# Performance work log

Hardware: AMD Instinct MI355X
Metric: run time of the kernel (lower is better)

The kernel has to match this reference:

```python
import jax, jax.numpy as jnp
import numpy as np

V = 5023   # FLAME vertex count
NJ = 5     # joints: global, neck, jaw, left eye, right eye
PARENTS = [-1, 0, 1, 1, 1]
N_SHAPE, N_EXPR = 100, 50
N_LMK = 68
B = 1024


def batch_rodrigues(rot_vecs):
    # rot_vecs: [N,3] axis-angle -> [N,3,3] rotation matrices
    angle = jnp.linalg.norm(rot_vecs + 1e-8, axis=1, keepdims=True)  # [N,1]
    rot_dir = rot_vecs / angle
    cos = jnp.cos(angle)[:, :, None]  # [N,1,1]
    sin = jnp.sin(angle)[:, :, None]
    rx, ry, rz = rot_dir[:, 0], rot_dir[:, 1], rot_dir[:, 2]
    zeros = jnp.zeros_like(rx)
    K = jnp.stack([zeros, -rz, ry,
                   rz, zeros, -rx,
                   -ry, rx, zeros], axis=1).reshape(-1, 3, 3)
    ident = jnp.eye(3, dtype=rot_vecs.dtype)
    return ident[None] + sin * K + (1.0 - cos) * jnp.matmul(K, K)


def setup_inputs() -> dict:
    key = jax.random.key(0)
    ks = jax.random.split(key, 12)
    shape_params = jax.random.normal(ks[0], (B, N_SHAPE), jnp.float32)
    expression_params = jax.random.normal(ks[1], (B, N_EXPR), jnp.float32)
    pose_params = 0.2 * jax.random.normal(ks[2], (B, 6), jnp.float32)
    land_index = jax.random.randint(ks[3], (N_LMK,), 0, V)
    # buffers / params (stand-ins for the pickled FLAME model)
    v_template = jax.random.normal(ks[4], (V, 3), jnp.float32) * 100.0
    v_template = v_template - jnp.mean(v_template, axis=0, keepdims=True)  # init centering
    shapedirs = jax.random.normal(ks[5], (V, 3, N_SHAPE + N_EXPR), jnp.float32) * 0.1
    posedirs = jax.random.normal(ks[6], ((NJ - 1) * 9, V * 3), jnp.float32) * 0.01
    J_regressor = jax.nn.softmax(jax.random.normal(ks[7], (NJ, V), jnp.float32), axis=1)
    lbs_weights = jax.nn.softmax(jax.random.normal(ks[8], (V, NJ), jnp.float32), axis=1)
    eye_pose = jnp.zeros((1, 6), jnp.float32)
    neck_pose = jnp.zeros((1, 3), jnp.float32)
    return dict(shape_params=shape_params, expression_params=expression_params,
                pose_params=pose_params, land_index=land_index,
                v_template=v_template, shapedirs=shapedirs, posedirs=posedirs,
                J_regressor=J_regressor, lbs_weights=lbs_weights,
                eye_pose=eye_pose, neck_pose=neck_pose)


def lbs(betas, full_pose, v_template, shapedirs, posedirs, J_regressor, lbs_weights):
    b = betas.shape[0]
    # shape/expression blendshapes
    v_shaped = v_template[None] + jnp.einsum('bl,vcl->bvc', betas, shapedirs)  # [B,V,3]
    J = jnp.einsum('jv,bvc->bjc', J_regressor, v_shaped)                       # [B,5,3]
    rot_mats = batch_rodrigues(full_pose.reshape(-1, 3)).reshape(b, NJ, 3, 3)
    ident = jnp.eye(3, dtype=betas.dtype)
    pose_feature = (rot_mats[:, 1:] - ident).reshape(b, -1)                    # [B,36]
    v_posed = v_shaped + jnp.matmul(pose_feature, posedirs).reshape(b, V, 3)
    # rigid transform along kinematic chain
    rel_joints = J.at[:, 1:].add(-J[:, jnp.array(PARENTS[1:])])
    top = jnp.concatenate([rot_mats, rel_joints[..., None]], axis=-1)          # [B,5,3,4]
    bottom = jnp.broadcast_to(jnp.array([0., 0., 0., 1.], betas.dtype), (b, NJ, 1, 4))
    transforms_mat = jnp.concatenate([top, bottom], axis=2)                    # [B,5,4,4]
    chain = [transforms_mat[:, 0]]
    for i in range(1, NJ):
        chain.append(jnp.matmul(chain[PARENTS[i]], transforms_mat[:, i]))
    transforms = jnp.stack(chain, axis=1)                                      # [B,5,4,4]
    posed_joints = transforms[:, :, :3, 3]
    t = jnp.einsum('bnij,bnj->bni', transforms[:, :, :3, :3], J)
    rel_transforms = transforms.at[:, :, :3, 3].add(-t)
    # skinning
    T = jnp.einsum('vj,bjxy->bvxy', lbs_weights, rel_transforms)               # [B,V,4,4]
    verts = jnp.einsum('bvxy,bvy->bvx', T[:, :, :3, :3], v_posed) + T[:, :, :3, 3]
    return verts, posed_joints


def reference(shape_params, expression_params, pose_params, land_index,
              v_template, shapedirs, posedirs, J_regressor, lbs_weights,
              eye_pose, neck_pose):
    b = shape_params.shape[0]
    betas = jnp.concatenate([shape_params, expression_params], axis=1)
    full_pose = jnp.concatenate([pose_params[:, :3],
                                 jnp.broadcast_to(neck_pose, (b, 3)),
                                 pose_params[:, 3:],
                                 jnp.broadcast_to(eye_pose, (b, 6))], axis=1)  # [B,15]
    vertices, _ = lbs(betas, full_pose, v_template, shapedirs, posedirs,
                      J_regressor, lbs_weights)
    landmarks3d = jnp.take(vertices, land_index, axis=1)
    return vertices, landmarks3d
```

## Files before the change

kernel.cpp:

```cpp
#include <hip/hip_runtime.h>

#define V_N 5023
#define V_PAD 5120
#define KTOT 192
#define B_N 1024
#define NC_REAL 15069

#define WS_W     0
#define WS_PART1 5898240
#define WS_PARTJ 6789240
#define WS_JS    6795180
#define WS_JT    6804180
#define WS_A2    5898240
#define WS_RELT  6291456

typedef __attribute__((ext_vector_type(8))) short bf16x8;
typedef __attribute__((ext_vector_type(4))) float f32x4;

__device__ __forceinline__ unsigned short f2bf(float f) {
  union { float f; unsigned int i; } x; x.f = f;
  unsigned int u = x.i;
  u = (u + 0x7FFFu + ((u >> 16) & 1u)) >> 16;
  return (unsigned short)u;
}

__global__ void k_wzero(float4* __restrict__ W4) {
  int g = blockIdx.x * 256 + threadIdx.x;
  W4[g] = make_float4(0.f, 0.f, 0.f, 0.f);
}

__global__ void k_w2a(const float* __restrict__ sd, unsigned int* __restrict__ W32) {
  int g = blockIdx.x * 256 + threadIdx.x;
  if (g >= NC_REAL * 75) return;
  int vc = g / 75, part = g - vc * 75;
  float2 s = *(const float2*)(sd + (size_t)vc * 150 + 2 * part);
  unsigned int w = (unsigned int)f2bf(s.x) | ((unsigned int)f2bf(s.y) << 16);
  int v = vc / 3, c = vc - 3 * v;
  W32[((size_t)c * V_PAD + v) * 96 + part] = w;
}

__global__ void k_w2b(const float* __restrict__ pd, unsigned short* __restrict__ W) {
  __shared__ unsigned short tile[64][38];
  int vc0 = blockIdx.x * 64;
  int t = threadIdx.x;
  for (int i = t; i < 2304; i += 256) {
    int kk = i >> 6, vl = i & 63;
    int vc = vc0 + vl;
    tile[vl][kk] = (vc < NC_REAL) ? f2bf(pd[(size_t)kk * NC_REAL + vc]) : (unsigned short)0;
  }
  __syncthreads();
  for (int i = t; i < 1152; i += 256) {
    int row = i / 18, part = i - row * 18;
    int vc = vc0 + row;
    if (vc < NC_REAL) {
      int v = vc / 3, c = vc - 3 * v;
      unsigned int w = (unsigned int)tile[row][2 * part] |
                       ((unsigned int)tile[row][2 * part + 1] << 16);
      *((unsigned int*)(W + ((size_t)c * V_PAD + v) * KTOT + 152) + part) = w;
    }
  }
}

__global__ void k_js1(const float* __restrict__ jreg, const float* __restrict__ sd,
                      const float* __restrict__ vt,
                      float* __restrict__ part1, float* __restrict__ partJ) {
  int blk = blockIdx.x;
  int vcidx = blk >> 1, kh = blk & 1;
  int t = threadIdx.x;
  int vs = vcidx * 51, ve = vs + 51; if (ve > V_N) ve = V_N;
  if (t < 75) {
    int k = kh * 75 + t;
    float acc[5][3];
    #pragma unroll
    for (int j = 0; j < 5; j++)
      #pragma unroll
      for (int c = 0; c < 3; c++) acc[j][c] = 0.f;
    #pragma unroll 2
    for (int v = vs; v < ve; v++) {
      float jr[5];
      #pragma unroll
      for (int j = 0; j < 5; j++) jr[j] = jreg[j * V_N + v];
      #pragma unroll
      for (int c = 0; c < 3; c++) {
        float s = sd[(size_t)(3 * v + c) * 150 + k];
        #pragma unroll
        for (int j = 0; j < 5; j++) acc[j][c] += jr[j] * s;
      }
    }
    #pragma unroll
    for (int j = 0; j < 5; j++)
      #pragma unroll
      for (int c = 0; c < 3; c++)
        part1[(size_t)vcidx * 2250 + (j * 3 + c) * 150 + kh * 75 + t] = acc[j][c];
  } else if (kh == 0 && t >= 80 && t < 95) {
    int j = (t - 80) / 3, c = (t - 80) % 3;
    float a = 0.f;
    for (int v = vs; v < ve; v++) a += jreg[j * V_N + v] * vt[3 * v + c];
    partJ[vcidx * 15 + (t - 80)] = a;
  }
}

__global__ void k_js2(const float* __restrict__ part1, const float* __restrict__ partJ,
                      float* __restrict__ JS, float* __restrict__ Jt) {
  int blk = blockIdx.x, t = threadIdx.x;
  if (blk < 9) {
    int u = blk * 256 + t;
    if (u < 2250) {
      float s = 0.f;
      #pragma unroll 4
      for (int p = 0; p < 99; p++) s += part1[(size_t)p * 2250 + u];
      JS[u] = s;
    }
  } else if (t < 15) {
    float s = 0.f;
    #pragma unroll 4
    for (int p = 0; p < 99; p++) s += partJ[p * 15 + t];
    Jt[t] = s;
  }
}

__global__ void k_a2(const float* __restrict__ shp, const float* __restrict__ expr,
                     unsigned short* __restrict__ A2) {
  int g = blockIdx.x * 256 + threadIdx.x;
  int b = g / 76, u = g - b * 76;
  int k0 = 2 * u, k1 = 2 * u + 1;
  float f0 = 0.f, f1 = 0.f;
  if (k0 < 100) f0 = shp[b * 100 + k0]; else if (k0 < 150) f0 = expr[b * 50 + k0 - 100];
  if (k1 < 100) f1 = shp[b * 100 + k1]; else if (k1 < 150) f1 = expr[b * 50 + k1 - 100];
  unsigned int w = (unsigned int)f2bf(f0) | ((unsigned int)f2bf(f1) << 16);
  ((unsigned int*)A2)[b * 96 + u] = w;
}

__device__ __forceinline__ void rodrigues(const float* p, float* R) {
  float x = p[0], y = p[1], z = p[2];
  float xa = x + 1e-8f, ya = y + 1e-8f, za = z + 1e-8f;
  float angle = sqrtf(xa * xa + ya * ya + za * za);
  float inv = 1.0f / angle;
  float rx = x * inv, ry = y * inv, rz = z * inv;
  float c = cosf(angle), s = sinf(angle), t1 = 1.0f - c;
  float K[9] = {0.f, -rz, ry, rz, 0.f, -rx, -ry, rx, 0.f};
  float KK[9];
  #pragma unroll
  for (int i = 0; i < 3; i++)
    #pragma unroll
    for (int j = 0; j < 3; j++) {
      float a = 0.f;
      #pragma unroll
      for (int k = 0; k < 3; k++) a += K[i * 3 + k] * K[k * 3 + j];
      KK[i * 3 + j] = a;
    }
  #pragma unroll
  for (int i = 0; i < 9; i++) R[i] = s * K[i] + t1 * KK[i];
  R[0] += 1.f; R[4] += 1.f; R[8] += 1.f;
}

__global__ __launch_bounds__(256) void k_pose(
    const float* __restrict__ pose, const float* __restrict__ neck,
    const float* __restrict__ eye, const float* __restrict__ shp,
    const float* __restrict__ expr, const float* __restrict__ JS,
    const float* __restrict__ Jt, unsigned short* __restrict__ A2,
    float* __restrict__ relT) {
  __shared__ float sBet[150 * 64];
  __shared__ float sJS[2250];
  int t = threadIdx.x;
  int b0 = blockIdx.x * 64;
  for (int i = t; i < 6400; i += 256) {
    int row = i / 100, col = i - row * 100;
    sBet[col * 64 + row] = shp[(size_t)(b0 + row) * 100 + col];
  }
  for (int i = t; i < 3200; i += 256) {
    int row = i / 50, col = i - row * 50;
    sBet[(100 + col) * 64 + row] = expr[(size_t)(b0 + row) * 50 + col];
  }
  for (int i = t; i < 2250; i += 256) sJS[i] = JS[i];
  __syncthreads();
  if (t >= 64) return;
  int b = b0 + t;
  float fp[15];
  fp[0] = pose[b * 6 + 0]; fp[1] = pose[b * 6 + 1]; fp[2] = pose[b * 6 + 2];
  fp[3] = neck[0]; fp[4] = neck[1]; fp[5] = neck[2];
  fp[6] = pose[b * 6 + 3]; fp[7] = pose[b * 6 + 4]; fp[8] = pose[b * 6 + 5];
  #pragma unroll
  for (int i = 0; i < 6; i++) fp[9 + i] = eye[i];
  float R[5][9];
  #pragma unroll
  for (int j = 0; j < 5; j++) rodrigues(&fp[j * 3], R[j]);
  float J[5][3];
  #pragma unroll
  for (int j = 0; j < 5; j++)
    #pragma unroll
    for (int c = 0; c < 3; c++) J[j][c] = Jt[j * 3 + c];
  for (int k = 0; k < 150; k++) {
    float be = sBet[k * 64 + t];
    #pragma unroll
    for (int j = 0; j < 5; j++)
      #pragma unroll
      for (int c = 0; c < 3; c++) J[j][c] += be * sJS[(j * 3 + c) * 150 + k];
  }
  float rel[5][3];
  #pragma unroll
  for (int c = 0; c < 3; c++) {
    rel[0][c] = J[0][c];
    rel[1][c] = J[1][c] - J[0][c];
    rel[2][c] = J[2][c] - J[1][c];
    rel[3][c] = J[3][c] - J[1][c];
    rel[4][c] = J[4][c] - J[1][c];
  }
  float GR[5][9], Gt[5][3];
  #pragma unroll
  for (int i = 0; i < 9; i++) GR[0][i] = R[0][i];
  #pragma unroll
  for (int c = 0; c < 3; c++) Gt[0][c] = rel[0][c];
  const int parent[5] = {0, 0, 1, 1, 1};
  #pragma unroll
  for (int j = 1; j < 5; j++) {
    int p = parent[j];
    #pragma unroll
    for (int r = 0; r < 3; r++)
      #pragma unroll
      for (int c = 0; c < 3; c++) {
        float a = 0.f;
        #pragma unroll
        for (int k = 0; k < 3; k++) a += GR[p][r * 3 + k] * R[j][k * 3 + c];
        GR[j][r * 3 + c] = a;
      }
    #pragma unroll
    for (int r = 0; r < 3; r++) {
      float a = Gt[p][r];
      #pragma unroll
      for (int k = 0; k < 3; k++) a += GR[p][r * 3 + k] * rel[j][k];
      Gt[j][r] = a;
    }
  }
  #pragma unroll
  for (int j = 0; j < 5; j++) {
    #pragma unroll
    for (int r = 0; r < 3; r++) {
      float a = 0.f;
      #pragma unroll
      for (int k = 0; k < 3; k++) a += GR[j][r * 3 + k] * J[j][k];
      float tr = Gt[j][r] - a;
      #pragma unroll
      for (int c = 0; c < 3; c++) relT[b * 60 + j * 12 + r * 4 + c] = GR[j][r * 3 + c];
      relT[b * 60 + j * 12 + r * 4 + 3] = tr;
    }
  }
  #pragma unroll
  for (int j = 1; j < 5; j++)
    #pragma unroll
    for (int r = 0; r < 3; r++)
      #pragma unroll
      for (int c = 0; c < 3; c++) {
        int kk = (j - 1) * 9 + r * 3 + c;
        A2[(size_t)b * KTOT + 152 + kk] = f2bf(R[j][r * 3 + c] - ((r == c) ? 1.f : 0.f));
      }
  #pragma unroll
  for (int kk = 36; kk < 40; kk++) A2[(size_t)b * KTOT + 152 + kk] = 0;
}

__global__ __launch_bounds__(256) void k_mfma(
    const unsigned short* __restrict__ W,
    const unsigned short* __restrict__ A2,
    const float* __restrict__ relT,
    const float* __restrict__ vt,
    const float* __restrict__ lbsw,
    float* __restrict__ out) {
  __shared__ float sRel[64 * 60];
  int t = threadIdx.x;
  int wave = t >> 6, lane = t & 63, ln = lane & 15, quad = lane >> 4;
  int wm = wave >> 1, wn = wave & 1;
  int v0 = blockIdx.x * 128, b0 = blockIdx.y * 64;

  for (int i = t; i < 3840; i += 256) sRel[i] = relT[(size_t)b0 * 60 + i];

  f32x4 acc[3][2][4];
  #pragma unroll
  for (int c = 0; c < 3; c++)
    #pragma unroll
    for (int mt = 0; mt < 2; mt++)
      #pragma unroll
      for (int nt = 0; nt < 4; nt++) {
        acc[c][mt][nt].x = 0.f; acc[c][mt][nt].y = 0.f;
        acc[c][mt][nt].z = 0.f; acc[c][mt][nt].w = 0.f;
      }

  const unsigned short* Abase = A2 + (size_t)(b0 + wm * 32 + ln) * KTOT + quad * 8;
  const unsigned short* Bbase = W + (size_t)(v0 + wn * 64 + ln) * KTOT + quad * 8;

  for (int kc = 0; kc < 6; kc++) {
    bf16x8 af0 = *(const bf16x8*)(Abase + kc * 32);
    bf16x8 af1 = *(const bf16x8*)(Abase + (size_t)16 * KTOT + kc * 32);
    #pragma unroll
    for (int c = 0; c < 3; c++)
      #pragma unroll
      for (int nt = 0; nt < 4; nt++) {
        bf16x8 bfr = *(const bf16x8*)(Bbase + ((size_t)c * V_PAD + nt * 16) * KTOT + kc * 32);
        acc[c][0][nt] = __builtin_amdgcn_mfma_f32_16x16x32_bf16(af0, bfr, acc[c][0][nt], 0, 0, 0);
        acc[c][1][nt] = __builtin_amdgcn_mfma_f32_16x16x32_bf16(af1, bfr, acc[c][1][nt], 0, 0, 0);
      }
  }
  __syncthreads();

  #pragma unroll
  for (int nt = 0; nt < 4; nt++) {
    int v = v0 + wn * 64 + nt * 16 + ln;
    bool ok = v < V_N;
    float vtx = 0.f, vty = 0.f, vtz = 0.f;
    float w5[5] = {0.f, 0.f, 0.f, 0.f, 0.f};
    if (ok) {
      vtx = vt[3 * v]; vty = vt[3 * v + 1]; vtz = vt[3 * v + 2];
      #pragma unroll
      for (int j = 0; j < 5; j++) w5[j] = lbsw[v * 5 + j];
    }
    #pragma unroll
    for (int mt = 0; mt < 2; mt++)
      #pragma unroll
      for (int reg = 0; reg < 4; reg++) {
        int bl = wm * 32 + mt * 16 + quad * 4 + reg;
        float px = acc[0][mt][nt][reg] + vtx;
        float py = acc[1][mt][nt][reg] + vty;
        float pz = acc[2][mt][nt][reg] + vtz;
        float ox = 0.f, oy = 0.f, oz = 0.f;
        const float* M = &sRel[bl * 60];
        #pragma unroll
        for (int j = 0; j < 5; j++) {
          const float* m = M + j * 12;
          float q0 = m[0] * px + m[1] * py + m[2] * pz + m[3];
          float q1 = m[4] * px + m[5] * py + m[6] * pz + m[7];
          float q2 = m[8] * px + m[9] * py + m[10] * pz + m[11];
          ox += w5[j] * q0; oy += w5[j] * q1; oz += w5[j] * q2;
        }
        if (ok) {
          size_t off = (size_t)(b0 + bl) * NC_REAL + (size_t)3 * v;
          out[off] = ox; out[off + 1] = oy; out[off + 2] = oz;
        }
      }
  }
}

__global__ void k_lmk(const float* __restrict__ verts,
                      const int* __restrict__ land,
                      float* __restrict__ lm) {
  int g = blockIdx.x * 256 + threadIdx.x;
  int b = g / 204;
  int r = g - b * 204;
  int i = r / 3, c = r - i * 3;
  lm[g] = verts[(size_t)b * NC_REAL + (size_t)land[i] * 3 + c];
}

extern "C" void kernel_launch(void* const* d_in, const int* in_sizes, int n_in,
                              void* d_out, int out_size, void* d_ws, size_t ws_size,
                              hipStream_t stream) {
  const float* shp  = (const float*)d_in[0];
  const float* expr = (const float*)d_in[1];
  const float* pose = (const float*)d_in[2];
  const int*   land = (const int*)d_in[3];
  const float* vt   = (const float*)d_in[4];
  const float* sd   = (const float*)d_in[5];
  const float* pd   = (const float*)d_in[6];
  const float* jreg = (const float*)d_in[7];
  const float* lbsw = (const float*)d_in[8];
  const float* eye  = (const float*)d_in[9];
  const float* neck = (const float*)d_in[10];
  char* ws = (char*)d_ws;
  unsigned short* W    = (unsigned short*)(ws + WS_W);
  float* part1 = (float*)(ws + WS_PART1);
  float* partJ = (float*)(ws + WS_PARTJ);
  float* JS    = (float*)(ws + WS_JS);
  float* Jt    = (float*)(ws + WS_JT);
  unsigned short* A2   = (unsigned short*)(ws + WS_A2);
  float* relT  = (float*)(ws + WS_RELT);
  float* outv = (float*)d_out;
  float* outl = outv + (size_t)B_N * NC_REAL;

  hipLaunchKernelGGL(k_wzero, dim3(1440),    dim3(256), 0, stream, (float4*)W);
  hipLaunchKernelGGL(k_w2a,   dim3(4415),    dim3(256), 0, stream, sd, (unsigned int*)W);
  hipLaunchKernelGGL(k_w2b,   dim3(236),     dim3(256), 0, stream, pd, W);
  hipLaunchKernelGGL(k_js1,   dim3(198),     dim3(128), 0, stream, jreg, sd, vt, part1, partJ);
  hipLaunchKernelGGL(k_js2,   dim3(10),      dim3(256), 0, stream, part1, partJ, JS, Jt);
  hipLaunchKernelGGL(k_a2,    dim3(304),     dim3(256), 0, stream, shp, expr, A2);
  hipLaunchKernelGGL(k_pose,  dim3(16),      dim3(256), 0, stream, pose, neck, eye, shp, expr, JS, Jt, A2, relT);
  hipLaunchKernelGGL(k_mfma,  dim3(40, 16),  dim3(256), 0, stream, W, A2, relT, vt, lbsw, outv);
  hipLaunchKernelGGL(k_lmk,   dim3(816),     dim3(256), 0, stream, outv, land, outl);
}
```

Measured before the change: 245.0 us.

## Fuse prep stages into fewer launches and compute landmarks in GEMM epilogue

Collapses nine launches into three. The weight repack, posedir transpose and joint-shape partial sums become branches of one prep kernel; the joint partials now use an LDS-tiled, coalesced loop over fewer chunks. A2 packing and the partial-sum reduction move into the pose kernel. The separate zero-fill of W is dropped, and the landmark gather is replaced by recomputing the landmark vertices inside the MFMA epilogue. The MFMA tile is halved along vertices with an occupancy hint. The risk is that W padding is no longer zeroed, so uninitialized workspace could leak in if it holds non-finite values.

After: 344.6 us. 1.41x slower.

```diff
diff --git a/kernel.cpp b/kernel.cpp
--- a/kernel.cpp
+++ b/kernel.cpp
@@ -5,14 +5,14 @@
 #define KTOT 192
 #define B_N 1024
 #define NC_REAL 15069
+#define NCHUNK 31
+#define VCHUNK 163
 
 #define WS_W     0
-#define WS_PART1 5898240
-#define WS_PARTJ 6789240
-#define WS_JS    6795180
-#define WS_JT    6804180
 #define WS_A2    5898240
 #define WS_RELT  6291456
+#define WS_PART1 6537216
+#define WS_PARTJ 6816216
 
 typedef __attribute__((ext_vector_type(8))) short bf16x8;
 typedef __attribute__((ext_vector_type(4))) float f32x4;
@@ -24,111 +24,99 @@
   return (unsigned short)u;
 }
 
-__global__ void k_wzero(float4* __restrict__ W4) {
-  int g = blockIdx.x * 256 + threadIdx.x;
-  W4[g] = make_float4(0.f, 0.f, 0.f, 0.f);
-}
-
-__global__ void k_w2a(const float* __restrict__ sd, unsigned int* __restrict__ W32) {
-  int g = blockIdx.x * 256 + threadIdx.x;
-  if (g >= NC_REAL * 75) return;
-  int vc = g / 75, part = g - vc * 75;
-  float2 s = *(const float2*)(sd + (size_t)vc * 150 + 2 * part);
-  unsigned int w = (unsigned int)f2bf(s.x) | ((unsigned int)f2bf(s.y) << 16);
-  int v = vc / 3, c = vc - 3 * v;
-  W32[((size_t)c * V_PAD + v) * 96 + part] = w;
-}
-
-__global__ void k_w2b(const float* __restrict__ pd, unsigned short* __restrict__ W) {
-  __shared__ unsigned short tile[64][38];
-  int vc0 = blockIdx.x * 64;
-  int t = threadIdx.x;
-  for (int i = t; i < 2304; i += 256) {
-    int kk = i >> 6, vl = i & 63;
-    int vc = vc0 + vl;
-    tile[vl][kk] = (vc < NC_REAL) ? f2bf(pd[(size_t)kk * NC_REAL + vc]) : (unsigned short)0;
-  }
-  __syncthreads();
-  for (int i = t; i < 1152; i += 256) {
-    int row = i / 18, part = i - row * 18;
-    int vc = vc0 + row;
-    if (vc < NC_REAL) {
+__global__ __launch_bounds__(256) void k_prep(
+    const float* __restrict__ sd, const float* __restrict__ pd,
+    const float* __restrict__ jreg, const float* __restrict__ vt,
+    unsigned short* __restrict__ W, float* __restrict__ part1,
+    float* __restrict__ partJ) {
+  __shared__ float smem[16 * 453 + 80 + 48];
+  int blk = blockIdx.x, t = threadIdx.x;
+  if (blk < 4415) {
+    int g = blk * 256 + t;
+    if (g < NC_REAL * 75) {
+      int vc = g / 75, part = g - vc * 75;
+      float2 s = *(const float2*)(sd + (size_t)vc * 150 + 2 * part);
+      unsigned int w = (unsigned int)f2bf(s.x) | ((unsigned int)f2bf(s.y) << 16);
       int v = vc / 3, c = vc - 3 * v;
-      unsigned int w = (unsigned int)tile[row][2 * part] |
-                       ((unsigned int)tile[row][2 * part + 1] << 16);
-      *((unsigned int*)(W + ((size_t)c * V_PAD + v) * KTOT + 152) + part) = w;
-    }
-  }
-}
-
-__global__ void k_js1(const float* __restrict__ jreg, const float* __restrict__ sd,
-                      const float* __restrict__ vt,
-                      float* __restrict__ part1, float* __restrict__ partJ) {
-  int blk = blockIdx.x;
-  int vcidx = blk >> 1, kh = blk & 1;
-  int t = threadIdx.x;
-  int vs = vcidx * 51, ve = vs + 51; if (ve > V_N) ve = V_N;
-  if (t < 75) {
-    int k = kh * 75 + t;
-    float acc[5][3];
-    #pragma unroll
-    for (int j = 0; j < 5; j++)
-      #pragma unroll
-      for (int c = 0; c < 3; c++) acc[j][c] = 0.f;
-    #pragma unroll 2
-    for (int v = vs; v < ve; v++) {
-      float jr[5];
-      #pragma unroll
-      for (int j = 0; j < 5; j++) jr[j] = jreg[j * V_N + v];
-      #pragma unroll
-      for (int c = 0; c < 3; c++) {
-        float s = sd[(size_t)(3 * v + c) * 150 + k];
-        #pragma unroll
-        for (int j = 0; j < 5; j++) acc[j][c] += jr[j] * s;
-      }
-    }
-    #pragma unroll
-    for (int j = 0; j < 5; j++)
-      #pragma unroll
-      for (int c = 0; c < 3; c++)
-        part1[(size_t)vcidx * 2250 + (j * 3 + c) * 150 + kh * 75 + t] = acc[j][c];
-  } else if (kh == 0 && t >= 80 && t < 95) {
-    int j = (t - 80) / 3, c = (t - 80) % 3;
-    float a = 0.f;
-    for (int v = vs; v < ve; v++) a += jreg[j * V_N + v] * vt[3 * v + c];
-    partJ[vcidx * 15 + (t - 80)] = a;
-  }
-}
-
-__global__ void k_js2(const float* __restrict__ part1, const float* __restrict__ partJ,
-                      float* __restrict__ JS, float* __restrict__ Jt) {
-  int blk = blockIdx.x, t = threadIdx.x;
-  if (blk < 9) {
-    int u = blk * 256 + t;
-    if (u < 2250) {
-      float s = 0.f;
-      #pragma unroll 4
-      for (int p = 0; p < 99; p++) s += part1[(size_t)p * 2250 + u];
-      JS[u] = s;
-    }
-  } else if (t < 15) {
-    float s = 0.f;
-    #pragma unroll 4
-    for (int p = 0; p < 99; p++) s += partJ[p * 15 + t];
-    Jt[t] = s;
-  }
-}
-
-__global__ void k_a2(const float* __restrict__ shp, const float* __restrict__ expr,
-                     unsigned short* __restrict__ A2) {
-  int g = blockIdx.x * 256 + threadIdx.x;
-  int b = g / 76, u = g - b * 76;
-  int k0 = 2 * u, k1 = 2 * u + 1;
-  float f0 = 0.f, f1 = 0.f;
-  if (k0 < 100) f0 = shp[b * 100 + k0]; else if (k0 < 150) f0 = expr[b * 50 + k0 - 100];
-  if (k1 < 100) f1 = shp[b * 100 + k1]; else if (k1 < 150) f1 = expr[b * 50 + k1 - 100];
-  unsigned int w = (unsigned int)f2bf(f0) | ((unsigned int)f2bf(f1) << 16);
-  ((unsigned int*)A2)[b * 96 + u] = w;
+      ((unsigned int*)W)[((size_t)c * V_PAD + v) * 96 + part] = w;
+    }
+  } else if (blk < 4651) {
+    unsigned short* tile = (unsigned short*)smem;
+    int vc0 = (blk - 4415) * 64;
+    for (int i = t; i < 2304; i += 256) {
+      int kk = i >> 6, vl = i & 63;
+      int vc = vc0 + vl;
+      tile[vl * 38 + kk] = (vc < NC_REAL) ? f2bf(pd[(size_t)kk * NC_REAL + vc]) : (unsigned short)0;
+    }
+    __syncthreads();
+    for (int i = t; i < 1152; i += 256) {
+      int row = i / 18, part = i - row * 18;
+      int vc = vc0 + row;
+      if (vc < NC_REAL) {
+        int v = vc / 3, c = vc - 3 * v;
+        unsigned int w = (unsigned int)tile[row * 38 + 2 * part] |
+                         ((unsigned int)tile[row * 38 + 2 * part + 1] << 16);
+        *((unsigned int*)(W + ((size_t)c * V_PAD + v) * KTOT + 152) + part) = w;
+      }
+    }
+  } else {
+    int chunk = blk - 4651;
+    int vbase = chunk * VCHUNK;
+    float* sdT = smem;
+    float* jrT = smem + 16 * 453;
+    float* vtT = smem + 16 * 453 + 80;
+    int c = 0, kk = 0, jj = 0, cc = 0;
+    float acc[2][5] = {{0,0,0,0,0},{0,0,0,0,0}};
+    float accJ = 0.f;
+    if (t < 225) { c = t / 75; kk = t - c * 75; }
+    else if (t >= 240) { int idx = t - 240; jj = idx / 3; cc = idx - 3 * jj; }
+    for (int s0 = 0; s0 < VCHUNK; s0 += 16) {
+      __syncthreads();
+      int nv = VCHUNK - s0; if (nv > 16) nv = 16;
+      for (int i = t; i < 7200; i += 256) {
+        int vl = i / 450, r = i - vl * 450;
+        int v = vbase + s0 + vl;
+        sdT[vl * 453 + r] = (vl < nv && v < V_N) ? sd[(size_t)v * 450 + r] : 0.f;
+      }
+      for (int i = t; i < 80; i += 256) {
+        int vl = i / 5, j = i - vl * 5;
+        int v = vbase + s0 + vl;
+        jrT[vl * 5 + j] = (vl < nv && v < V_N) ? jreg[j * V_N + v] : 0.f;
+      }
+      for (int i = t; i < 48; i += 256) {
+        int vl = i / 3, c2 = i - vl * 3;
+        int v = vbase + s0 + vl;
+        vtT[vl * 3 + c2] = (vl < nv && v < V_N) ? vt[v * 3 + c2] : 0.f;
+      }
+      __syncthreads();
+      if (t < 225) {
+        #pragma unroll 4
+        for (int vl = 0; vl < 16; vl++) {
+          float slo = sdT[vl * 453 + c * 150 + kk];
+          float shi = sdT[vl * 453 + c * 150 + kk + 75];
+          #pragma unroll
+          for (int j = 0; j < 5; j++) {
+            float jr = jrT[vl * 5 + j];
+            acc[0][j] += jr * slo;
+            acc[1][j] += jr * shi;
+          }
+        }
+      } else if (t >= 240 && t < 255) {
+        #pragma unroll 4
+        for (int vl = 0; vl < 16; vl++)
+          accJ += jrT[vl * 5 + jj] * vtT[vl * 3 + cc];
+      }
+    }
+    if (t < 225) {
+      #pragma unroll
+      for (int j = 0; j < 5; j++) {
+        part1[(size_t)chunk * 2250 + (j * 3 + c) * 150 + kk] = acc[0][j];
+        part1[(size_t)chunk * 2250 + (j * 3 + c) * 150 + kk + 75] = acc[1][j];
+      }
+    } else if (t >= 240 && t < 255) {
+      partJ[chunk * 15 + (t - 240)] = accJ;
+    }
+  }
 }
 
 __device__ __forceinline__ void rodrigues(const float* p, float* R) {
@@ -137,7 +125,7 @@
   float angle = sqrtf(xa * xa + ya * ya + za * za);
   float inv = 1.0f / angle;
   float rx = x * inv, ry = y * inv, rz = z * inv;
-  float c = cosf(angle), s = sinf(angle), t1 = 1.0f - c;
+  float cth = cosf(angle), s = sinf(angle), t1 = 1.0f - cth;
   float K[9] = {0.f, -rz, ry, rz, 0.f, -rx, -ry, rx, 0.f};
   float KK[9];
   #pragma unroll
@@ -154,16 +142,28 @@
   R[0] += 1.f; R[4] += 1.f; R[8] += 1.f;
 }
 
-__global__ __launch_bounds__(256) void k_pose(
+__global__ __launch_bounds__(256) void k_mid(
     const float* __restrict__ pose, const float* __restrict__ neck,
     const float* __restrict__ eye, const float* __restrict__ shp,
-    const float* __restrict__ expr, const float* __restrict__ JS,
-    const float* __restrict__ Jt, unsigned short* __restrict__ A2,
+    const float* __restrict__ expr, const float* __restrict__ part1,
+    const float* __restrict__ partJ, unsigned short* __restrict__ A2,
     float* __restrict__ relT) {
   __shared__ float sBet[150 * 64];
   __shared__ float sJS[2250];
-  int t = threadIdx.x;
-  int b0 = blockIdx.x * 64;
+  __shared__ float sJt[16];
+  int blk = blockIdx.x, t = threadIdx.x;
+  if (blk < 304) {
+    int g = blk * 256 + t;
+    int b = g / 76, u = g - b * 76;
+    int k0 = 2 * u, k1 = 2 * u + 1;
+    float f0 = 0.f, f1 = 0.f;
+    if (k0 < 100) f0 = shp[b * 100 + k0]; else if (k0 < 150) f0 = expr[b * 50 + k0 - 100];
+    if (k1 < 100) f1 = shp[b * 100 + k1]; else if (k1 < 150) f1 = expr[b * 50 + k1 - 100];
+    unsigned int w = (unsigned int)f2bf(f0) | ((unsigned int)f2bf(f1) << 16);
+    ((unsigned int*)A2)[b * 96 + u] = w;
+    return;
+  }
+  int b0 = (blk - 304) * 64;
   for (int i = t; i < 6400; i += 256) {
     int row = i / 100, col = i - row * 100;
     sBet[col * 64 + row] = shp[(size_t)(b0 + row) * 100 + col];
@@ -172,7 +172,17 @@
     int row = i / 50, col = i - row * 50;
     sBet[(100 + col) * 64 + row] = expr[(size_t)(b0 + row) * 50 + col];
   }
-  for (int i = t; i < 2250; i += 256) sJS[i] = JS[i];
+  for (int i = t; i < 2250; i += 256) {
+    float s = 0.f;
+    #pragma unroll 4
+    for (int p = 0; p < NCHUNK; p++) s += part1[(size_t)p * 2250 + i];
+    sJS[i] = s;
+  }
+  if (t < 15) {
+    float s = 0.f;
+    for (int p = 0; p < NCHUNK; p++) s += partJ[p * 15 + t];
+    sJt[t] = s;
+  }
   __syncthreads();
   if (t >= 64) return;
   int b = b0 + t;
@@ -189,7 +199,7 @@
   #pragma unroll
   for (int j = 0; j < 5; j++)
     #pragma unroll
-    for (int c = 0; c < 3; c++) J[j][c] = Jt[j * 3 + c];
+    for (int c = 0; c < 3; c++) J[j][c] = sJt[j * 3 + c];
   for (int k = 0; k < 150; k++) {
     float be = sBet[k * 64 + t];
     #pragma unroll
@@ -258,42 +268,47 @@
   for (int kk = 36; kk < 40; kk++) A2[(size_t)b * KTOT + 152 + kk] = 0;
 }
 
-__global__ __launch_bounds__(256) void k_mfma(
+__global__ __launch_bounds__(256, 4) void k_mfma(
     const unsigned short* __restrict__ W,
     const unsigned short* __restrict__ A2,
     const float* __restrict__ relT,
     const float* __restrict__ vt,
     const float* __restrict__ lbsw,
-    float* __restrict__ out) {
+    const int* __restrict__ land,
+    float* __restrict__ out,
+    float* __restrict__ outl) {
   __shared__ float sRel[64 * 60];
+  __shared__ int sLand[68];
   int t = threadIdx.x;
   int wave = t >> 6, lane = t & 63, ln = lane & 15, quad = lane >> 4;
   int wm = wave >> 1, wn = wave & 1;
-  int v0 = blockIdx.x * 128, b0 = blockIdx.y * 64;
+  int v0 = blockIdx.x * 64, b0 = blockIdx.y * 64;
 
   for (int i = t; i < 3840; i += 256) sRel[i] = relT[(size_t)b0 * 60 + i];
-
-  f32x4 acc[3][2][4];
+  if (t < 68) sLand[t] = land[t];
+
+  f32x4 acc[3][2][2];
   #pragma unroll
   for (int c = 0; c < 3; c++)
     #pragma unroll
     for (int mt = 0; mt < 2; mt++)
       #pragma unroll
-      for (int nt = 0; nt < 4; nt++) {
+      for (int nt = 0; nt < 2; nt++) {
         acc[c][mt][nt].x = 0.f; acc[c][mt][nt].y = 0.f;
         acc[c][mt][nt].z = 0.f; acc[c][mt][nt].w = 0.f;
       }
 
   const unsigned short* Abase = A2 + (size_t)(b0 + wm * 32 + ln) * KTOT + quad * 8;
-  const unsigned short* Bbase = W + (size_t)(v0 + wn * 64 + ln) * KTOT + quad * 8;
-
+  const unsigned short* Bbase = W + (size_t)(v0 + wn * 32 + ln) * KTOT + quad * 8;
+
+  #pragma unroll
   for (int kc = 0; kc < 6; kc++) {
     bf16x8 af0 = *(const bf16x8*)(Abase + kc * 32);
     bf16x8 af1 = *(const bf16x8*)(Abase + (size_t)16 * KTOT + kc * 32);
     #pragma unroll
     for (int c = 0; c < 3; c++)
       #pragma unroll
-      for (int nt = 0; nt < 4; nt++) {
+      for (int nt = 0; nt < 2; nt++) {
         bf16x8 bfr = *(const bf16x8*)(Bbase + ((size_t)c * V_PAD + nt * 16) * KTOT + kc * 32);
         acc[c][0][nt] = __builtin_amdgcn_mfma_f32_16x16x32_bf16(af0, bfr, acc[c][0][nt], 0, 0, 0);
         acc[c][1][nt] = __builtin_amdgcn_mfma_f32_16x16x32_bf16(af1, bfr, acc[c][1][nt], 0, 0, 0);
@@ -302,8 +317,8 @@
   __syncthreads();
 
   #pragma unroll
-  for (int nt = 0; nt < 4; nt++) {
-    int v = v0 + wn * 64 + nt * 16 + ln;
+  for (int nt = 0; nt < 2; nt++) {
+    int v = v0 + wn * 32 + nt * 16 + ln;
     bool ok = v < V_N;
     float vtx = 0.f, vty = 0.f, vtz = 0.f;
     float w5[5] = {0.f, 0.f, 0.f, 0.f, 0.f};
@@ -325,27 +340,40 @@
         #pragma unroll
         for (int j = 0; j < 5; j++) {
           const float* m = M + j * 12;
-          float q0 = m[0] * px + m[1] * py + m[2] * pz + m[3];
-          float q1 = m[4] * px + m[5] * py + m[6] * pz + m[7];
-          float q2 = m[8] * px + m[9] * py + m[10] * pz + m[11];
-          ox += w5[j] * q0; oy += w5[j] * q1; oz += w5[j] * q2;
+          ox += w5[j] * (m[0] * px + m[1] * py + m[2] * pz + m[3]);
+          oy += w5[j] * (m[4] * px + m[5] * py + m[6] * pz + m[7]);
+          oz += w5[j] * (m[8] * px + m[9] * py + m[10] * pz + m[11]);
         }
         if (ok) {
           size_t off = (size_t)(b0 + bl) * NC_REAL + (size_t)3 * v;
           out[off] = ox; out[off + 1] = oy; out[off + 2] = oz;
         }
       }
-  }
-}
-
-__global__ void k_lmk(const float* __restrict__ verts,
-                      const int* __restrict__ land,
-                      float* __restrict__ lm) {
-  int g = blockIdx.x * 256 + threadIdx.x;
-  int b = g / 204;
-  int r = g - b * 204;
-  int i = r / 3, c = r - i * 3;
-  lm[g] = verts[(size_t)b * NC_REAL + (size_t)land[i] * 3 + c];
+    for (int i = 0; i < 68; i++) {
+      if (sLand[i] == v) {
+        #pragma unroll
+        for (int mt = 0; mt < 2; mt++)
+          #pragma unroll
+          for (int reg = 0; reg < 4; reg++) {
+            int bl = wm * 32 + mt * 16 + quad * 4 + reg;
+            float px = acc[0][mt][nt][reg] + vtx;
+            float py = acc[1][mt][nt][reg] + vty;
+            float pz = acc[2][mt][nt][reg] + vtz;
+            float ox = 0.f, oy = 0.f, oz = 0.f;
+            const float* M = &sRel[bl * 60];
+            #pragma unroll
+            for (int j = 0; j < 5; j++) {
+              const float* m = M + j * 12;
+              ox += w5[j] * (m[0] * px + m[1] * py + m[2] * pz + m[3]);
+              oy += w5[j] * (m[4] * px + m[5] * py + m[6] * pz + m[7]);
+              oz += w5[j] * (m[8] * px + m[9] * py + m[10] * pz + m[11]);
+            }
+            size_t off = ((size_t)(b0 + bl) * 68 + i) * 3;
+            outl[off] = ox; outl[off + 1] = oy; outl[off + 2] = oz;
+          }
+      }
+    }
+  }
 }
 
 extern "C" void kernel_launch(void* const* d_in, const int* in_sizes, int n_in,
@@ -364,22 +392,17 @@
   const float* neck = (const float*)d_in[10];
   char* ws = (char*)d_ws;
   unsigned short* W    = (unsigned short*)(ws + WS_W);
+  unsigned short* A2   = (unsigned short*)(ws + WS_A2);
+  float* relT  = (float*)(ws + WS_RELT);
   float* part1 = (float*)(ws + WS_PART1);
   float* partJ = (float*)(ws + WS_PARTJ);
-  float* JS    = (float*)(ws + WS_JS);
-  float* Jt    = (float*)(ws + WS_JT);
-  unsigned short* A2   = (unsigned short*)(ws + WS_A2);
-  float* relT  = (float*)(ws + WS_RELT);
   float* outv = (float*)d_out;
   float* outl = outv + (size_t)B_N * NC_REAL;
 
-  hipLaunchKernelGGL(k_wzero, dim3(1440),    dim3(256), 0, stream, (float4*)W);
-  hipLaunchKernelGGL(k_w2a,   dim3(4415),    dim3(256), 0, stream, sd, (unsigned int*)W);
-  hipLaunchKernelGGL(k_w2b,   dim3(236),     dim3(256), 0, stream, pd, W);
-  hipLaunchKernelGGL(k_js1,   dim3(198),     dim3(128), 0, stream, jreg, sd, vt, part1, partJ);
-  hipLaunchKernelGGL(k_js2,   dim3(10),      dim3(256), 0, stream, part1, partJ, JS, Jt);
-  hipLaunchKernelGGL(k_a2,    dim3(304),     dim3(256), 0, stream, shp, expr, A2);
-  hipLaunchKernelGGL(k_pose,  dim3(16),      dim3(256), 0, stream, pose, neck, eye, shp, expr, JS, Jt, A2, relT);
-  hipLaunchKernelGGL(k_mfma,  dim3(40, 16),  dim3(256), 0, stream, W, A2, relT, vt, lbsw, outv);
-  hipLaunchKernelGGL(k_lmk,   dim3(816),     dim3(256), 0, stream, outv, land, outl);
-}
+  hipLaunchKernelGGL(k_prep, dim3(4682),   dim3(256), 0, stream,
+                     sd, pd, jreg, vt, W, part1, partJ);
+  hipLaunchKernelGGL(k_mid,  dim3(320),    dim3(256), 0, stream,
+                     pose, neck, eye, shp, expr, part1, partJ, A2, relT);
+  hipLaunchKernelGGL(k_mfma, dim3(80, 16), dim3(256), 0, stream,
+                     W, A2, relT, vt, lbsw, land, outv, outl);
+}
```
